# Kernel optimization log

Measured on AMD Instinct MI355X. Metric: run time of the kernel, lower is better.

## Reference

```python
import jax, jax.numpy as jnp
import numpy as np

D = 384        # model dim
H = 6          # heads
HD = 64        # head dim (inner_dim = H*HD = 384)
DEPTH = 12
P = 16         # patch size
G = 14         # grid side (224/16)
NP = G * G     # 196 patches
NC = 1000
B = 64
DFF = 4 * D
SCALE = HD ** -0.5
EPS = 1e-5


def _ln(x, w, b):
    m = x.mean(-1, keepdims=True)
    v = ((x - m) ** 2).mean(-1, keepdims=True)
    return (x - m) * jax.lax.rsqrt(v + EPS) * w + b


def setup_inputs() -> dict:
    key = jax.random.key(0)
    ks = jax.random.split(key, 16)
    s = 0.02
    inp = {
        "x": jax.random.normal(ks[0], (B, 3, 224, 224), jnp.float32),
        # patch embedding conv as matmul: weight [3*P*P, D]
        "W_patch": jax.random.normal(ks[1], (3 * P * P, D), jnp.float32) * s,
        "b_patch": jnp.zeros((D,), jnp.float32),
        "ln0_w": jnp.ones((D,), jnp.float32),
        "ln0_b": jnp.zeros((D,), jnp.float32),
        "pos_emb": jax.random.normal(ks[2], (1, NP + 1, D), jnp.float32) * s,
        "cls_token": jax.random.normal(ks[3], (1, D), jnp.float32),
        # per-block params stacked over depth
        "ln1_w": jnp.ones((DEPTH, D), jnp.float32),
        "ln1_b": jnp.zeros((DEPTH, D), jnp.float32),
        "Wq": jax.random.normal(ks[4], (DEPTH, D, H * HD), jnp.float32) * s,
        "Wkv": jax.random.normal(ks[5], (DEPTH, D, 2 * H * HD), jnp.float32) * s,
        "Wo": jax.random.normal(ks[6], (DEPTH, H * HD, D), jnp.float32) * s,
        "bo": jnp.zeros((DEPTH, D), jnp.float32),
        "ln2_w": jnp.ones((DEPTH, D), jnp.float32),
        "ln2_b": jnp.zeros((DEPTH, D), jnp.float32),
        "W1": jax.random.normal(ks[7], (DEPTH, D, DFF), jnp.float32) * s,
        "b1": jnp.zeros((DEPTH, DFF), jnp.float32),
        "W2": jax.random.normal(ks[8], (DEPTH, DFF, D), jnp.float32) * s,
        "b2": jnp.zeros((DEPTH, D), jnp.float32),
        "lnf_w": jnp.ones((D,), jnp.float32),
        "lnf_b": jnp.zeros((D,), jnp.float32),
        "Whead": jax.random.normal(ks[9], (D, NC), jnp.float32) * s,
        "bhead": jnp.zeros((NC,), jnp.float32),
    }
    return inp


def reference(x, W_patch, b_patch, ln0_w, ln0_b, pos_emb, cls_token,
              ln1_w, ln1_b, Wq, Wkv, Wo, bo, ln2_w, ln2_b,
              W1, b1, W2, b2, lnf_w, lnf_b, Whead, bhead):
    b = x.shape[0]
    # patch embed: Conv2d(3, D, P, stride=P) == extract patches + matmul
    patches = x.reshape(b, 3, G, P, G, P).transpose(0, 2, 4, 1, 3, 5).reshape(b, NP, 3 * P * P)
    h = patches @ W_patch + b_patch                     # [b, NP, D]
    h = _ln(h, ln0_w, ln0_b)
    cls = jnp.broadcast_to(cls_token[None], (b, 1, D))
    h = jnp.concatenate([cls, h], axis=1) + pos_emb     # [b, NP+1, D]
    n = NP + 1
    for d in range(DEPTH):
        # self-attention with pre-LN, residual
        a = _ln(h, ln1_w[d], ln1_b[d])
        q = (a @ Wq[d]).reshape(b, n, H, HD).transpose(0, 2, 1, 3)
        kv = a @ Wkv[d]
        k = kv[..., : H * HD].reshape(b, n, H, HD).transpose(0, 2, 1, 3)
        v = kv[..., H * HD:].reshape(b, n, H, HD).transpose(0, 2, 1, 3)
        sim = jnp.einsum('bhid,bhjd->bhij', q, k) * SCALE
        attn = jax.nn.softmax(sim, axis=-1)
        o = jnp.einsum('bhij,bhjd->bhid', attn, v)
        o = o.transpose(0, 2, 1, 3).reshape(b, n, H * HD)
        h = h + o @ Wo[d] + bo[d]
        # MLP with pre-LN, residual, exact GELU
        m = _ln(h, ln2_w[d], ln2_b[d])
        m = jax.nn.gelu(m @ W1[d] + b1[d], approximate=False)
        h = h + m @ W2[d] + b2[d]
    cls_out = h[:, 0, :]
    logits = _ln(cls_out, lnf_w, lnf_b) @ Whead + bhead
    return logits
```

## Files before the change

kernel.cpp:

```cpp
#include <hip/hip_runtime.h>


typedef unsigned short u16;
typedef __attribute__((ext_vector_type(8))) short short8;
typedef __attribute__((ext_vector_type(4))) float f32x4;
typedef __attribute__((ext_vector_type(4))) unsigned short u16x4;
typedef __attribute__((ext_vector_type(2))) unsigned short u16x2;

#define D_      384
#define NH      6
#define DEPTH_  12
#define NP_     196
#define NT_     197
#define B_      64
#define DFF_    1536
#define M_REAL  (B_*NT_)
#define M_PAD   12800
#define M_PATCH (B_*NP_)

__device__ __forceinline__ float bf2f(u16 u){
  unsigned int i = ((unsigned int)u) << 16;
  return __builtin_bit_cast(float, i);
}
__device__ __forceinline__ u16 f2bf(float f){
  unsigned int i = __builtin_bit_cast(unsigned int, f);
  i = (i + 0x7FFFu + ((i >> 16) & 1u)) >> 16;
  return (u16)i;
}
__device__ __forceinline__ float gelu_f(float x){
  float t = x * (1.595769122f + 0.0713548162726f * x * x);
  return x / (1.f + __expf(-t));
}

#define GLOAD_LDS16(g, l) __builtin_amdgcn_global_load_lds( \
    (const __attribute__((address_space(1))) void*)(g),      \
    (__attribute__((address_space(3))) void*)(l), 16, 0, 0)

#define MFMA_BF16(a, b, c) __builtin_amdgcn_mfma_f32_16x16x32_bf16((a), (b), (c), 0, 0, 0)

struct TJobs {
  const float* src[7];
  u16*         dst[7];
  int          N[7], K[7], Nsrc[7];
  long long    ss[7], ds[7];
  int          cnt[7];
};

__global__ __launch_bounds__(256) void transpose_all(TJobs J)
{
  __shared__ float tile[32][33];
  int local = blockIdx.x;
  int j = 0;
  while (local >= J.cnt[j]) { local -= J.cnt[j]; ++j; }
  int nbx = J.N[j] >> 5, nby = J.K[j] >> 5;
  int z   = local / (nbx * nby);
  int rem = local - z * nbx * nby;
  int by = rem / nbx, bx = rem - by * nbx;
  const float* src = J.src[j] + (long long)z * J.ss[j];
  u16* dst = J.dst[j] + (long long)z * J.ds[j];
  int K = J.K[j], Nsrc = J.Nsrc[j];
  int tx = threadIdx.x, ty = threadIdx.y;
  int n0 = bx * 32, k0 = by * 32;
#pragma unroll
  for (int i = 0; i < 4; ++i){
    float v = 0.f;
    if (n0 + tx < Nsrc) v = src[(size_t)(k0 + ty + i*8) * Nsrc + n0 + tx];
    tile[ty + i*8][tx] = v;
  }
  __syncthreads();
#pragma unroll
  for (int i = 0; i < 4; ++i)
    dst[(size_t)(n0 + ty + i*8) * K + k0 + tx] = f2bf(tile[tx][ty + i*8]);
}

__global__ __launch_bounds__(256) void patch_extract(const float* __restrict__ x,
                                                     u16* __restrict__ patches)
{
  int r = blockIdx.x;
  int b = r / NP_, p = r % NP_;
  int gy = p / 14, gx = p % 14;
  int t = threadIdx.x;
  int py = t >> 4, px = t & 15;
#pragma unroll
  for (int c = 0; c < 3; ++c){
    float v = x[(((size_t)b*3 + c)*224 + gy*16 + py)*224 + gx*16 + px];
    patches[(size_t)r*768 + c*256 + t] = f2bf(v);
  }
}

template<int MODE, int BM, int BN, int KS, int NW>
__global__ __launch_bounds__(NW*64) void gemm_k(const u16* __restrict__ A,
                                                const u16* __restrict__ Bt,
                                                const float* __restrict__ bias,
                                                u16* __restrict__ outb,
                                                float* __restrict__ outf,
                                                int N, int K, int nbx, size_t sstride)
{
  constexpr int WAVES_M = (NW == 8) ? 4 : 2;
  constexpr int WM = BM / WAVES_M;
  constexpr int WN = BN / 2;
  constexpr int MI = WM / 16;
  constexpr int NJ = WN / 16;
  constexpr int CA = BM / (16 * NW);
  constexpr int CB = BN / (16 * NW);
  constexpr int L  = CA + CB;
  __shared__ u16 lds[2*(BM+BN)*32];
  u16* As = lds;
  u16* Bs = lds + 2*BM*32;
  int tid = threadIdx.x;
  int w = tid >> 6, lane = tid & 63;

  int nwg = gridDim.x;
  int q = nwg >> 3, r = nwg & 7;
  int xcd = blockIdx.x & 7, slot = blockIdx.x >> 3;
  int wgid = (xcd < r ? xcd*(q+1) : r*(q+1) + (xcd - r)*q) + slot;
  int m0 = (wgid / nbx) * BM;
  int n0 = (wgid % nbx) * BN;
  int kz = (KS > 1) ? blockIdx.y : 0;
  int Kl = K / KS;
  int koff = kz * Kl;
  int wr = w >> 1, wc = w & 1;

  f32x4 acc[MI][NJ];
#pragma unroll
  for (int i = 0; i < MI; ++i)
#pragma unroll
    for (int j = 0; j < NJ; ++j) acc[i][j] = (f32x4){0.f,0.f,0.f,0.f};

  int srow = lane >> 2;
  int skc  = ((lane & 3) ^ ((lane >> 3) & 3)) * 8;
  const u16* Ag = A  + (size_t)(m0 + w*16 + srow) * K + koff + skc;
  const u16* Bg = Bt + (size_t)(n0 + w*16 + srow) * K + koff + skc;

  int fr  = lane & 15;
  int fsw = ((lane >> 4) ^ ((lane >> 1) & 3)) << 3;

  auto stage = [&](int bi, int kt){
    u16* Ad = As + bi*(BM*32) + (w*16)*32;
    u16* Bd = Bs + bi*(BN*32) + (w*16)*32;
#pragma unroll
    for (int c = 0; c < CA; ++c)
      GLOAD_LDS16(Ag + (size_t)(c*16*NW)*K + kt, Ad + c*16*NW*32);
#pragma unroll
    for (int c = 0; c < CB; ++c)
      GLOAD_LDS16(Bg + (size_t)(c*16*NW)*K + kt, Bd + c*16*NW*32);
  };
  auto compute = [&](int bi){
    const u16* Ab = As + bi*(BM*32);
    const u16* Bb = Bs + bi*(BN*32);
    short8 af[MI], bfr[NJ];
#pragma unroll
    for (int i = 0; i < MI; ++i)
      af[i]  = *(const short8*)&Ab[(wr*WM + i*16 + fr)*32 + fsw];
#pragma unroll
    for (int j = 0; j < NJ; ++j)
      bfr[j] = *(const short8*)&Bb[(wc*WN + j*16 + fr)*32 + fsw];
#pragma unroll
    for (int i = 0; i < MI; ++i)
#pragma unroll
      for (int j = 0; j < NJ; ++j)
        acc[i][j] = MFMA_BF16(af[i], bfr[j], acc[i][j]);
  };

#define WAIT_L()  do { \
    if constexpr (L == 2)      asm volatile("s_waitcnt vmcnt(2)" ::: "memory"); \
    else if constexpr (L == 3) asm volatile("s_waitcnt vmcnt(3)" ::: "memory"); \
    else                       asm volatile("s_waitcnt vmcnt(4)" ::: "memory"); \
  } while (0)

  int nk = Kl >> 5;
  stage(0, 0);
  for (int t = 0; t < nk; t += 2){
    stage(1, (t + 1) * 32);
    __builtin_amdgcn_sched_barrier(0);
    WAIT_L();
    __builtin_amdgcn_s_barrier();
    asm volatile("" ::: "memory");
    compute(0);
    __builtin_amdgcn_sched_barrier(0);
    __builtin_amdgcn_s_barrier();
    if (t + 2 < nk){
      stage(0, (t + 2) * 32);
      __builtin_amdgcn_sched_barrier(0);
      WAIT_L();
    } else {
      __builtin_amdgcn_sched_barrier(0);
      asm volatile("s_waitcnt vmcnt(0)" ::: "memory");
    }
    __builtin_amdgcn_s_barrier();
    asm volatile("" ::: "memory");
    compute(1);
    __builtin_amdgcn_sched_barrier(0);
    __builtin_amdgcn_s_barrier();
  }
#undef WAIT_L

  int cr = (lane >> 4) << 2;
  int cc = lane & 15;

  if constexpr (MODE == 3){
#pragma unroll
    for (int j = 0; j < NJ; ++j){
      int c = n0 + wc*WN + j*16 + cc;
      float bv = bias ? bias[c] : 0.f;
#pragma unroll
      for (int i = 0; i < MI; ++i){
        int rbase = m0 + wr*WM + i*16 + cr;
#pragma unroll
        for (int e = 0; e < 4; ++e){
          float v = acc[i][j][e] + bv;
          if (c < N) outf[(size_t)(rbase + e) * N + c] = v;
        }
      }
    }
  } else {
    constexpr int PITCH = WN + 8;
    u16* Cs = lds + w * (16 * PITCH);
    u16* outp = (MODE == 4) ? outb + (size_t)kz * sstride : outb;
    int lr0 = lane >> 3;
    int lc  = lane & 7;
#pragma unroll
    for (int i = 0; i < MI; ++i){
#pragma unroll
      for (int j = 0; j < NJ; ++j){
        int c = n0 + wc*WN + j*16 + cc;
        float bv = (bias && kz == 0) ? bias[c] : 0.f;
#pragma unroll
        for (int e = 0; e < 4; ++e){
          float v = acc[i][j][e] + bv;
          if (MODE == 2) v = gelu_f(v);
          Cs[(cr + e) * PITCH + j*16 + cc] = f2bf(v);
        }
      }
#pragma unroll
      for (int p = 0; p < 2; ++p){
        int lr = p*8 + lr0;
        short8 val = *(const short8*)&Cs[lr * PITCH + lc*8];
        size_t gm = (size_t)(m0 + wr*WM + i*16 + lr);
        *(short8*)&outp[gm * N + n0 + wc*WN + lc*8] = val;
      }
    }
  }
}

__global__ __launch_bounds__(256) void ln_rows(const float* __restrict__ in,
                                               const float* __restrict__ gw,
                                               const float* __restrict__ gb,
                                               u16* __restrict__ out, int rows,
                                               size_t rstride)
{
  int m = blockIdx.x * 4 + (threadIdx.x >> 6);
  int lane = threadIdx.x & 63;
  if (m >= rows) return;
  const float* r = in + (size_t)m * rstride;
  float4 v0 = *(const float4*)(r + lane*4);
  float2 v1 = *(const float2*)(r + 256 + lane*2);
  float sum = v0.x+v0.y+v0.z+v0.w+v1.x+v1.y;
  float sq  = v0.x*v0.x+v0.y*v0.y+v0.z*v0.z+v0.w*v0.w+v1.x*v1.x+v1.y*v1.y;
#pragma unroll
  for (int d = 1; d < 64; d <<= 1){ sum += __shfl_xor(sum, d); sq += __shfl_xor(sq, d); }
  float mean = sum * (1.f/D_);
  float rs = rsqrtf(sq*(1.f/D_) - mean*mean + 1e-5f);
  float4 w0 = *(const float4*)(gw + lane*4);
  float2 w1 = *(const float2*)(gw + 256 + lane*2);
  float4 b0 = *(const float4*)(gb + lane*4);
  float2 b1v= *(const float2*)(gb + 256 + lane*2);
  u16x4 o4 = { f2bf((v0.x-mean)*rs*w0.x + b0.x), f2bf((v0.y-mean)*rs*w0.y + b0.y),
               f2bf((v0.z-mean)*rs*w0.z + b0.z), f2bf((v0.w-mean)*rs*w0.w + b0.w) };
  u16x2 o2 = { f2bf((v1.x-mean)*rs*w1.x + b1v.x), f2bf((v1.y-mean)*rs*w1.y + b1v.y) };
  *(u16x4*)(out + (size_t)m*D_ + lane*4) = o4;
  *(u16x2*)(out + (size_t)m*D_ + 256 + lane*2) = o2;
}

__global__ __launch_bounds__(256) void ln_rows_add(const float* __restrict__ in,
                                                   const u16* __restrict__ s0,
                                                   const u16* __restrict__ s1,
                                                   const float* __restrict__ gw,
                                                   const float* __restrict__ gb,
                                                   u16* __restrict__ out,
                                                   float* __restrict__ hout,
                                                   int rows, size_t rstride)
{
  int m = blockIdx.x * 4 + (threadIdx.x >> 6);
  int lane = threadIdx.x & 63;
  if (m >= rows) return;
  const float* r = in + (size_t)m * rstride;
  const u16* p0 = s0 + (size_t)m * rstride;
  const u16* p1 = s1 + (size_t)m * rstride;
  float4 v0 = *(const float4*)(r + lane*4);
  float2 v1 = *(const float2*)(r + 256 + lane*2);
  u16x4 a0 = *(const u16x4*)(p0 + lane*4);
  u16x2 a1 = *(const u16x2*)(p0 + 256 + lane*2);
  u16x4 c0 = *(const u16x4*)(p1 + lane*4);
  u16x2 c1 = *(const u16x2*)(p1 + 256 + lane*2);
  float x0 = v0.x + bf2f(a0.x) + bf2f(c0.x);
  float x1 = v0.y + bf2f(a0.y) + bf2f(c0.y);
  float x2 = v0.z + bf2f(a0.z) + bf2f(c0.z);
  float x3 = v0.w + bf2f(a0.w) + bf2f(c0.w);
  float x4 = v1.x + bf2f(a1.x) + bf2f(c1.x);
  float x5 = v1.y + bf2f(a1.y) + bf2f(c1.y);
  float sum = x0+x1+x2+x3+x4+x5;
  float sq  = x0*x0+x1*x1+x2*x2+x3*x3+x4*x4+x5*x5;
#pragma unroll
  for (int d = 1; d < 64; d <<= 1){ sum += __shfl_xor(sum, d); sq += __shfl_xor(sq, d); }
  float mean = sum * (1.f/D_);
  float rs = rsqrtf(sq*(1.f/D_) - mean*mean + 1e-5f);
  float4 w0 = *(const float4*)(gw + lane*4);
  float2 w1 = *(const float2*)(gw + 256 + lane*2);
  float4 b0 = *(const float4*)(gb + lane*4);
  float2 b1v= *(const float2*)(gb + 256 + lane*2);
  u16x4 o4 = { f2bf((x0-mean)*rs*w0.x + b0.x), f2bf((x1-mean)*rs*w0.y + b0.y),
               f2bf((x2-mean)*rs*w0.z + b0.z), f2bf((x3-mean)*rs*w0.w + b0.w) };
  u16x2 o2 = { f2bf((x4-mean)*rs*w1.x + b1v.x), f2bf((x5-mean)*rs*w1.y + b1v.y) };
  *(u16x4*)(out + (size_t)m*D_ + lane*4) = o4;
  *(u16x2*)(out + (size_t)m*D_ + 256 + lane*2) = o2;
  if (hout){
    float* ho = hout + (size_t)m * rstride;
    float4 h0 = {x0,x1,x2,x3};
    float2 h1 = {x4,x5};
    *(float4*)(ho + lane*4) = h0;
    *(float2*)(ho + 256 + lane*2) = h1;
  }
}

__global__ __launch_bounds__(256) void assemble_h(const u16* __restrict__ pe,
                                                  const float* __restrict__ gw,
                                                  const float* __restrict__ gb,
                                                  const float* __restrict__ pos,
                                                  const float* __restrict__ cls,
                                                  float* __restrict__ h)
{
  int m = blockIdx.x * 4 + (threadIdx.x >> 6);
  int lane = threadIdx.x & 63;
  if (m >= M_PAD) return;
  float* ho = h + (size_t)m * D_;
  if (m >= M_REAL){
    float4 z = {0.f,0.f,0.f,0.f};
    *(float4*)(ho + lane*4) = z;
    float2 z2 = {0.f,0.f};
    *(float2*)(ho + 256 + lane*2) = z2;
    return;
  }
  int b = m / NT_, t = m % NT_;
  const float* pr = pos + (size_t)t * D_;
  float4 p0 = *(const float4*)(pr + lane*4);
  float2 p1 = *(const float2*)(pr + 256 + lane*2);
  if (t == 0){
    float4 c0 = *(const float4*)(cls + lane*4);
    float2 c1 = *(const float2*)(cls + 256 + lane*2);
    float4 r0 = {c0.x+p0.x, c0.y+p0.y, c0.z+p0.z, c0.w+p0.w};
    float2 r1 = {c1.x+p1.x, c1.y+p1.y};
    *(float4*)(ho + lane*4) = r0;
    *(float2*)(ho + 256 + lane*2) = r1;
  } else {
    const u16* per = pe + (size_t)(b*NP_ + (t-1)) * D_;
    u16x4 a0 = *(const u16x4*)(per + lane*4);
    u16x2 a1 = *(const u16x2*)(per + 256 + lane*2);
    float x0=bf2f(a0.x), x1=bf2f(a0.y), x2=bf2f(a0.z), x3=bf2f(a0.w), x4=bf2f(a1.x), x5=bf2f(a1.y);
    float sum = x0+x1+x2+x3+x4+x5;
    float sq  = x0*x0+x1*x1+x2*x2+x3*x3+x4*x4+x5*x5;
#pragma unroll
    for (int d = 1; d < 64; d <<= 1){ sum += __shfl_xor(sum, d); sq += __shfl_xor(sq, d); }
    float mean = sum * (1.f/D_);
    float rs = rsqrtf(sq*(1.f/D_) - mean*mean + 1e-5f);
    float4 w0 = *(const float4*)(gw + lane*4);
    float2 w1 = *(const float2*)(gw + 256 + lane*2);
    float4 b0 = *(const float4*)(gb + lane*4);
    float2 b1v= *(const float2*)(gb + 256 + lane*2);
    float4 r0 = { (x0-mean)*rs*w0.x + b0.x + p0.x, (x1-mean)*rs*w0.y + b0.y + p0.y,
                  (x2-mean)*rs*w0.z + b0.z + p0.z, (x3-mean)*rs*w0.w + b0.w + p0.w };
    float2 r1 = { (x4-mean)*rs*w1.x + b1v.x + p1.x, (x5-mean)*rs*w1.y + b1v.y + p1.y };
    *(float4*)(ho + lane*4) = r0;
    *(float2*)(ho + 256 + lane*2) = r1;
  }
}

__global__ __launch_bounds__(256) void attn_k(const u16* __restrict__ qkv,
                                              u16* __restrict__ o)
{
  __shared__ u16 Ks[208*72];
  __shared__ u16 Vt[64*232];
  __shared__ u16 Ps[4][16*40];
  int bh = blockIdx.x;
  int b = bh / NH, hh = bh % NH;
  int tid = threadIdx.x, w = tid >> 6, lane = tid & 63;
  const u16* kbase = qkv + (size_t)b*NT_*1152 + 384 + hh*64;
  const u16* vbase = kbase + 384;

  int jr = tid >> 3, col = (tid & 7) * 8;
#pragma unroll
  for (int it = 0; it < 7; ++it){
    int j = it*32 + jr;
    if (j < 208){
      uint4 val = {0u,0u,0u,0u};
      if (j < 197) val = *(const uint4*)(kbase + (size_t)j*1152 + col);
      *(uint4*)&Ks[j*72 + col] = val;
    }
  }
#pragma unroll
  for (int it = 0; it < 7; ++it){
    int j = it*32 + jr;
    union { uint4 v; u16 s[8]; } u;
    u.v.x = 0u; u.v.y = 0u; u.v.z = 0u; u.v.w = 0u;
    if (j < 197) u.v = *(const uint4*)(vbase + (size_t)j*1152 + col);
#pragma unroll
    for (int e = 0; e < 8; ++e) Vt[(size_t)(col+e)*232 + j] = u.s[e];
  }
  __syncthreads();

  u16* myP = Ps[w];
  int fr = lane & 15, fk = lane >> 4;

  for (int qt = w; qt < 13; qt += 4){
    const u16* qrow = qkv + (size_t)(b*NT_ + qt*16 + fr)*1152 + hh*64 + fk*8;
    short8 aq0 = *(const short8*)qrow;
    short8 aq1 = *(const short8*)(qrow + 32);

    f32x4 s[13];
#pragma unroll
    for (int jt = 0; jt < 13; ++jt){
      const u16* kr = &Ks[(jt*16 + fr)*72 + fk*8];
      short8 bk0 = *(const short8*)kr;
      short8 bk1 = *(const short8*)(kr + 32);
      f32x4 z = {0.f,0.f,0.f,0.f};
      z = MFMA_BF16(aq0, bk0, z);
      z = MFMA_BF16(aq1, bk1, z);
      s[jt] = z;
    }

#pragma unroll
    for (int e = 0; e < 4; ++e){
      float mx = -1e30f;
#pragma unroll
      for (int jt = 0; jt < 13; ++jt){
        int cj = jt*16 + fr;
        float v = (cj < NT_) ? s[jt][e]*0.125f : -1e30f;
        s[jt][e] = v;
        mx = fmaxf(mx, v);
      }
#pragma unroll
      for (int d = 1; d < 16; d <<= 1) mx = fmaxf(mx, __shfl_xor(mx, d));
      float su = 0.f;
#pragma unroll
      for (int jt = 0; jt < 13; ++jt){
        float p = __expf(s[jt][e] - mx);
        s[jt][e] = p; su += p;
      }
#pragma unroll
      for (int d = 1; d < 16; d <<= 1) su += __shfl_xor(su, d);
      float ri = 1.f / su;
#pragma unroll
      for (int jt = 0; jt < 13; ++jt) s[jt][e] *= ri;
    }

    f32x4 oacc[4];
#pragma unroll
    for (int dt = 0; dt < 4; ++dt) oacc[dt] = (f32x4){0.f,0.f,0.f,0.f};
#pragma unroll
    for (int jc = 0; jc < 7; ++jc){
#pragma unroll
      for (int jtl = 0; jtl < 2; ++jtl){
        int jt = jc*2 + jtl;
#pragma unroll
        for (int e = 0; e < 4; ++e){
          u16 pv = 0;
          if (jt < 13) pv = f2bf(s[jt][e]);
          myP[(fk*4 + e)*40 + jtl*16 + fr] = pv;
        }
      }
      asm volatile("s_waitcnt lgkmcnt(0)" ::: "memory");
      short8 pa = *(const short8*)&myP[fr*40 + fk*8];
#pragma unroll
      for (int dt = 0; dt < 4; ++dt){
        short8 bv = *(const short8*)&Vt[(size_t)(dt*16 + fr)*232 + jc*32 + fk*8];
        oacc[dt] = MFMA_BF16(pa, bv, oacc[dt]);
      }
    }

#pragma unroll
    for (int dt = 0; dt < 4; ++dt)
#pragma unroll
      for (int e = 0; e < 4; ++e){
        int t = qt*16 + fk*4 + e;
        if (t < NT_)
          o[(size_t)(b*NT_ + t)*384 + hh*64 + dt*16 + fr] = f2bf(oacc[dt][e]);
      }
  }
}

extern "C" void kernel_launch(void* const* d_in, const int* in_sizes, int n_in,
                              void* d_out, int out_size, void* d_ws, size_t ws_size,
                              hipStream_t stream)
{
  (void)in_sizes; (void)n_in; (void)out_size; (void)ws_size;
  const float* x_in    = (const float*)d_in[0];
  const float* W_patch = (const float*)d_in[1];
  const float* b_patch = (const float*)d_in[2];
  const float* ln0_w   = (const float*)d_in[3];
  const float* ln0_b   = (const float*)d_in[4];
  const float* pos_emb = (const float*)d_in[5];
  const float* cls_tok = (const float*)d_in[6];
  const float* ln1_w   = (const float*)d_in[7];
  const float* ln1_b   = (const float*)d_in[8];
  const float* Wq      = (const float*)d_in[9];
  const float* Wkv     = (const float*)d_in[10];
  const float* Wo      = (const float*)d_in[11];
  const float* bo      = (const float*)d_in[12];
  const float* ln2_w   = (const float*)d_in[13];
  const float* ln2_b   = (const float*)d_in[14];
  const float* W1      = (const float*)d_in[15];
  const float* b1      = (const float*)d_in[16];
  const float* W2      = (const float*)d_in[17];
  const float* b2      = (const float*)d_in[18];
  const float* lnf_w   = (const float*)d_in[19];
  const float* lnf_b   = (const float*)d_in[20];
  const float* Whead   = (const float*)d_in[21];
  const float* bhead   = (const float*)d_in[22];

  char* ws = (char*)d_ws;
  size_t off = 0;
  auto nxt = [&](size_t bytes)->char* {
    char* p = ws + off;
    off += (bytes + 255) & ~(size_t)255;
    return p;
  };
  u16*   g_buf   = (u16*)  nxt((size_t)M_PAD * DFF_ * 2);
  float* hbuf    = (float*)nxt((size_t)M_PAD * D_ * 4);
  u16*   abuf    = (u16*)  nxt((size_t)M_PAD * D_ * 2);
  u16*   qkvbuf  = (u16*)  nxt((size_t)M_PAD * 1152 * 2);
  u16*   obuf    = (u16*)  nxt((size_t)M_PAD * D_ * 2);
  u16*   sbuf    = (u16*)  nxt((size_t)2 * M_PAD * D_ * 2);
  u16*   lncls   = (u16*)  nxt((size_t)B_ * D_ * 2);
  u16*   whT     = (u16*)  nxt((size_t)1024 * D_ * 2);
  u16*   wT      = (u16*)  nxt((size_t)21528576 * 2);

  const size_t SS = (size_t)M_PAD * D_;
  u16* patches = g_buf;
  u16* pebuf   = abuf;
  u16* wpT   = wT;
  u16* wqkvT = wpT   + 294912;
  u16* woT   = wqkvT + 12*442368;
  u16* w1T   = woT   + 12*147456;
  u16* w2T   = w1T   + 12*589824;

  TJobs J;
  auto setj = [&](int i, const float* s, u16* d, int N, int K, int Nsrc,
                  long long ss, long long ds, int nz){
    J.src[i]=s; J.dst[i]=d; J.N[i]=N; J.K[i]=K; J.Nsrc[i]=Nsrc;
    J.ss[i]=ss; J.ds[i]=ds; J.cnt[i]=(N/32)*(K/32)*nz;
  };
  setj(0, W_patch, wpT,             384,  768,  384, 0, 0, 1);
  setj(1, Wq,      wqkvT,           384,  384,  384, 384LL*384,  1152LL*384, 12);
  setj(2, Wkv,     wqkvT + 384*384, 768,  384,  768, 384LL*768,  1152LL*384, 12);
  setj(3, Wo,      woT,             384,  384,  384, 384LL*384,  384LL*384,  12);
  setj(4, W1,      w1T,             1536, 384, 1536, 384LL*1536, 384LL*1536, 12);
  setj(5, W2,      w2T,             384, 1536,  384, 1536LL*384, 1536LL*384, 12);
  setj(6, Whead,   whT,             1024, 384, 1000, 0, 0, 1);
  int tblocks = 0;
  for (int i = 0; i < 7; ++i) tblocks += J.cnt[i];
  transpose_all<<<tblocks, dim3(32,8), 0, stream>>>(J);

  patch_extract<<<M_PATCH, 256, 0, stream>>>(x_in, patches);
  gemm_k<0,128,128,1,8><<<3*(M_PATCH/128), 512, 0, stream>>>(patches, wpT, b_patch, pebuf, nullptr, 384, 768, 3, 0);
  assemble_h<<<M_PAD/4, 256, 0, stream>>>(pebuf, ln0_w, ln0_b, pos_emb, cls_tok, hbuf);

  for (int d = 0; d < DEPTH_; ++d){
    if (d == 0)
      ln_rows<<<M_PAD/4, 256, 0, stream>>>(hbuf, ln1_w, ln1_b, abuf, M_PAD, D_);
    else
      ln_rows_add<<<M_PAD/4, 256, 0, stream>>>(hbuf, sbuf, sbuf + SS,
                                               ln1_w + d*384, ln1_b + d*384,
                                               abuf, hbuf, M_PAD, D_);
    gemm_k<0,256,128,1,8><<<9*(M_PAD/256), 512, 0, stream>>>(abuf, wqkvT + (size_t)d*442368, nullptr, qkvbuf, nullptr, 1152, 384, 9, 0);
    attn_k<<<B_*NH, 256, 0, stream>>>(qkvbuf, obuf);
    gemm_k<4,256,128,2,8><<<dim3(3*(M_PAD/256), 2), 512, 0, stream>>>(obuf, woT + (size_t)d*147456, bo + d*384, sbuf, nullptr, 384, 384, 3, SS);
    ln_rows_add<<<M_PAD/4, 256, 0, stream>>>(hbuf, sbuf, sbuf + SS,
                                             ln2_w + d*384, ln2_b + d*384,
                                             abuf, hbuf, M_PAD, D_);
    gemm_k<2,256,128,1,8><<<12*(M_PAD/256), 512, 0, stream>>>(abuf, w1T + (size_t)d*589824, b1 + d*1536, g_buf, nullptr, 1536, 384, 12, 0);
    gemm_k<4,256,128,2,8><<<dim3(3*(M_PAD/256), 2), 512, 0, stream>>>(g_buf, w2T + (size_t)d*589824, b2 + d*384, sbuf, nullptr, 384, 1536, 3, SS);
  }

  ln_rows_add<<<B_/4, 256, 0, stream>>>(hbuf, sbuf, sbuf + SS,
                                        lnf_w, lnf_b, lncls, nullptr,
                                        B_, (size_t)NT_*D_);
  gemm_k<3,64,64,1,4><<<16, 256, 0, stream>>>(lncls, whT, bhead, nullptr, (float*)d_out, 1000, 384, 16, 0);
}
```

Measured before the change: 1.834 ms.

## Add B-stationary GEMM keeping weight stripe in LDS across multiple M tiles

After: 4.017 ms. 2.19x slower.

```diff
diff --git a/kernel.cpp b/kernel.cpp
--- a/kernel.cpp
+++ b/kernel.cpp
@@ -85,6 +85,109 @@
   for (int c = 0; c < 3; ++c){
     float v = x[(((size_t)b*3 + c)*224 + gy*16 + py)*224 + gx*16 + px];
     patches[(size_t)r*768 + c*256 + t] = f2bf(v);
+  }
+}
+
+template<int MODE, int KL, int KS>
+__global__ __launch_bounds__(512, 4) void gemm_bs(const u16* __restrict__ A,
+                                                  const u16* __restrict__ Bt,
+                                                  const float* __restrict__ bias,
+                                                  u16* __restrict__ outb,
+                                                  int N, int K, int nstripes,
+                                                  int Mtiles, int mpg, size_t sstride)
+{
+  constexpr int BN  = 64;
+  constexpr int MI  = 4;
+  constexpr int NJ  = 2;
+  constexpr int NCH = KL / 8;
+  constexpr int NK  = KL / 32;
+  constexpr int PITCH = 40;
+  __shared__ u16 Bs[BN * KL];
+  __shared__ u16 Cs[8 * 16 * PITCH];
+
+  int tid = threadIdx.x, w = tid >> 6, lane = tid & 63;
+
+  int nwg = gridDim.x;
+  int q = nwg >> 3, r = nwg & 7;
+  int xcd = blockIdx.x & 7, slot = blockIdx.x >> 3;
+  int wgid = (xcd < r ? xcd*(q+1) : r*(q+1) + (xcd - r)*q) + slot;
+  int g  = wgid / nstripes;
+  int ns = wgid - g * nstripes;
+  int n0 = ns * BN;
+  int kz = (KS > 1) ? blockIdx.y : 0;
+  int koff = kz * KL;
+
+  int wr = w >> 1, wc = w & 1;
+  int fr = lane & 15, fk = lane >> 4;
+  int frs = fr & 7;
+
+  constexpr int ROUNDS = (BN * NCH) / 512;
+#pragma unroll
+  for (int rd = 0; rd < ROUNDS; ++rd){
+    int idx = rd*512 + tid;
+    int row = idx / NCH;
+    int pos = idx - row * NCH;
+    int sc  = (pos & ~7) | ((pos & 7) ^ (row & 7));
+    GLOAD_LDS16(Bt + (size_t)(n0 + row) * K + koff + sc*8, Bs + (size_t)idx * 8);
+  }
+  __syncthreads();
+
+  int rb0 = wc*32 + fr;
+  u16* Cw = Cs + w * (16 * PITCH);
+  u16* outp = (MODE == 4) ? outb + (size_t)kz * sstride : outb;
+  int cr = (lane >> 4) << 2;
+  int cc = lane & 15;
+  int lr = lane >> 2, lc = lane & 3;
+
+  for (int mt = 0; mt < mpg; ++mt){
+    int m_tile = g * mpg + mt;
+    if (m_tile >= Mtiles) break;
+    int m0 = m_tile * 256;
+
+    f32x4 acc[MI][NJ];
+#pragma unroll
+    for (int i = 0; i < MI; ++i)
+#pragma unroll
+      for (int j = 0; j < NJ; ++j) acc[i][j] = (f32x4){0.f,0.f,0.f,0.f};
+
+    const u16* Ab = A + (size_t)(m0 + wr*64 + fr) * K + koff + fk*8;
+
+#pragma unroll
+    for (int t = 0; t < NK; ++t){
+      short8 av[MI];
+#pragma unroll
+      for (int i = 0; i < MI; ++i)
+        av[i] = *(const short8*)(Ab + (size_t)(i*16) * K + t*32);
+      short8 bv[NJ];
+      int c  = t*4 + fk;
+      int p  = (c & ~7) | ((c & 7) ^ frs);
+#pragma unroll
+      for (int j = 0; j < NJ; ++j)
+        bv[j] = *(const short8*)&Bs[(rb0 + j*16) * KL + p*8];
+#pragma unroll
+      for (int i = 0; i < MI; ++i)
+#pragma unroll
+        for (int j = 0; j < NJ; ++j)
+          acc[i][j] = MFMA_BF16(av[i], bv[j], acc[i][j]);
+    }
+
+#pragma unroll
+    for (int i = 0; i < MI; ++i){
+#pragma unroll
+      for (int j = 0; j < NJ; ++j){
+        int ccol = n0 + wc*32 + j*16 + cc;
+        float bv_ = (bias && kz == 0) ? bias[ccol] : 0.f;
+#pragma unroll
+        for (int e = 0; e < 4; ++e){
+          float v = acc[i][j][e] + bv_;
+          if (MODE == 2) v = gelu_f(v);
+          Cw[(cr + e) * PITCH + j*16 + cc] = f2bf(v);
+        }
+      }
+      short8 val = *(const short8*)&Cw[lr * PITCH + lc*8];
+      size_t gm = (size_t)(m0 + wr*64 + i*16 + lr);
+      *(short8*)&outp[gm * N + n0 + wc*32 + lc*8] = val;
+    }
   }
 }
 
@@ -216,7 +319,7 @@
   } else {
     constexpr int PITCH = WN + 8;
     u16* Cs = lds + w * (16 * PITCH);
-    u16* outp = (MODE == 4) ? outb + (size_t)kz * sstride : outb;
+    u16* outp = outb;
     int lr0 = lane >> 3;
     int lc  = lane & 7;
 #pragma unroll
@@ -234,9 +337,9 @@
       }
 #pragma unroll
       for (int p = 0; p < 2; ++p){
-        int lr = p*8 + lr0;
-        short8 val = *(const short8*)&Cs[lr * PITCH + lc*8];
-        size_t gm = (size_t)(m0 + wr*WM + i*16 + lr);
+        int lrr = p*8 + lr0;
+        short8 val = *(const short8*)&Cs[lrr * PITCH + lc*8];
+        size_t gm = (size_t)(m0 + wr*WM + i*16 + lrr);
         *(short8*)&outp[gm * N + n0 + wc*WN + lc*8] = val;
       }
     }
@@ -564,6 +667,7 @@
   gemm_k<0,128,128,1,8><<<3*(M_PATCH/128), 512, 0, stream>>>(patches, wpT, b_patch, pebuf, nullptr, 384, 768, 3, 0);
   assemble_h<<<M_PAD/4, 256, 0, stream>>>(pebuf, ln0_w, ln0_b, pos_emb, cls_tok, hbuf);
 
+  const int MT = M_PAD / 256;
   for (int d = 0; d < DEPTH_; ++d){
     if (d == 0)
       ln_rows<<<M_PAD/4, 256, 0, stream>>>(hbuf, ln1_w, ln1_b, abuf, M_PAD, D_);
@@ -571,14 +675,14 @@
       ln_rows_add<<<M_PAD/4, 256, 0, stream>>>(hbuf, sbuf, sbuf + SS,
                                                ln1_w + d*384, ln1_b + d*384,
                                                abuf, hbuf, M_PAD, D_);
-    gemm_k<0,256,128,1,8><<<9*(M_PAD/256), 512, 0, stream>>>(abuf, wqkvT + (size_t)d*442368, nullptr, qkvbuf, nullptr, 1152, 384, 9, 0);
+    gemm_bs<0,384,1><<<dim3(18*17,1), 512, 0, stream>>>(abuf, wqkvT + (size_t)d*442368, nullptr, qkvbuf, 1152, 384, 18, MT, 3, 0);
     attn_k<<<B_*NH, 256, 0, stream>>>(qkvbuf, obuf);
-    gemm_k<4,256,128,2,8><<<dim3(3*(M_PAD/256), 2), 512, 0, stream>>>(obuf, woT + (size_t)d*147456, bo + d*384, sbuf, nullptr, 384, 384, 3, SS);
+    gemm_bs<4,192,2><<<dim3(6*25,2), 512, 0, stream>>>(obuf, woT + (size_t)d*147456, bo + d*384, sbuf, 384, 384, 6, MT, 2, SS);
     ln_rows_add<<<M_PAD/4, 256, 0, stream>>>(hbuf, sbuf, sbuf + SS,
                                              ln2_w + d*384, ln2_b + d*384,
                                              abuf, hbuf, M_PAD, D_);
-    gemm_k<2,256,128,1,8><<<12*(M_PAD/256), 512, 0, stream>>>(abuf, w1T + (size_t)d*589824, b1 + d*1536, g_buf, nullptr, 1536, 384, 12, 0);
-    gemm_k<4,256,128,2,8><<<dim3(3*(M_PAD/256), 2), 512, 0, stream>>>(g_buf, w2T + (size_t)d*589824, b2 + d*384, sbuf, nullptr, 384, 1536, 3, SS);
+    gemm_bs<2,384,1><<<dim3(24*17,1), 512, 0, stream>>>(abuf, w1T + (size_t)d*589824, b1 + d*1536, g_buf, 1536, 384, 24, MT, 3, 0);
+    gemm_bs<4,768,2><<<dim3(6*25,2), 512, 0, stream>>>(g_buf, w2T + (size_t)d*589824, b2 + d*384, sbuf, 384, 1536, 6, MT, 2, SS);
   }
 
   ln_rows_add<<<B_/4, 256, 0, stream>>>(hbuf, sbuf, sbuf + SS,
```
